# Optimization experiments

Measured on AMD Instinct MI355X. Metric: run time of the kernel, lower is better.

The kernel has to match this reference:

```python
import jax, jax.numpy as jnp
import numpy as np

IN_DIM = 128
OUT_DIM = 128
N_NEIGH = 32
BATCH = 8192


def setup_inputs() -> dict:
    key = jax.random.key(0)
    k1, k2, k3, k4, k5 = jax.random.split(key, 5)
    ai_sq = jax.random.normal(k1, (BATCH, IN_DIM), dtype=jnp.float32)
    ai_sn = jax.random.normal(k2, (N_NEIGH, BATCH, IN_DIM), dtype=jnp.float32)
    # nn.Linear params (weight [out,in], bias [out]) and attention vector u [2*out]
    W_w = jax.random.normal(k3, (OUT_DIM, IN_DIM), dtype=jnp.float32) / np.sqrt(IN_DIM)
    W_b = jax.random.normal(k4, (OUT_DIM,), dtype=jnp.float32) * 0.01
    u = jax.random.normal(k5, (2 * OUT_DIM,), dtype=jnp.float32)
    return {"ai_sq": ai_sq, "ai_sn": ai_sn, "W_w": W_w, "W_b": W_b, "u": u}


def reference(ai_sq, ai_sn, W_w, W_b, u):
    out_dim = W_w.shape[0]
    # shared linear projection W
    sq_proj = ai_sq @ W_w.T + W_b                      # [B, D]
    sn_proj = jnp.einsum('nbi,oi->nbo', ai_sn, W_w) + W_b  # [N, B, D]
    # u . concat(sq_proj, sn_proj) == u1.sq_proj + u2.sn_proj
    u1, u2 = u[:out_dim], u[out_dim:]
    mult = (sq_proj @ u1)[None, :] + jnp.einsum('nbd,d->nb', sn_proj, u2)  # [N, B]
    beta = jnp.exp(jax.nn.leaky_relu(mult, negative_slope=0.01))           # [N, B]
    return beta / jnp.sum(beta, axis=0)                # softmax-like normalize over neighbors
```

## Files before the change

### kernel.cpp

```cpp
#include <hip/hip_runtime.h>
#include <math.h>

#define IN_DIM   128
#define OUT_DIM  128
#define N_NEIGH  32
#define BATCH    8192

__global__ __launch_bounds__(128) void prep_kernel(const float* __restrict__ W_w,
                                                   const float* __restrict__ W_b,
                                                   const float* __restrict__ u,
                                                   float* __restrict__ ws) {
    int i = threadIdx.x;
    float a1 = 0.f, a2 = 0.f;
    for (int o = 0; o < OUT_DIM; ++o) {
        float w = W_w[o * IN_DIM + i];
        a1 += w * u[o];
        a2 += w * u[OUT_DIM + o];
    }
    ws[i] = a1;
    ws[IN_DIM + i] = a2;

    __shared__ float red[128];
    red[i] = W_b[i] * (u[i] + u[OUT_DIM + i]);
    __syncthreads();
    for (int s = 64; s > 0; s >>= 1) {
        if (i < s) red[i] += red[i + s];
        __syncthreads();
    }
    if (i == 0) ws[2 * IN_DIM] = red[0];
}

__global__ __launch_bounds__(256) void gat_kernel(const float* __restrict__ ai_sq,
                                                  const float* __restrict__ ai_sn,
                                                  const float* __restrict__ ws,
                                                  float* __restrict__ out) {
    const int b    = blockIdx.x;
    const int tid  = threadIdx.x;
    const int half = tid >> 5;
    const int c    = tid & 31;

    __shared__ float t[33];

    const float4* v1 = (const float4*)ws;
    const float4* v2 = (const float4*)(ws + IN_DIM);
    const float   cc = ws[2 * IN_DIM];

    const float4 v2c = v2[c];

    for (int r = half; r < 33; r += 8) {
        float4 x, vv;
        if (r < 32) {
            x  = ((const float4*)(ai_sn + ((size_t)r * BATCH + b) * IN_DIM))[c];
            vv = v2c;
        } else {
            x  = ((const float4*)(ai_sq + (size_t)b * IN_DIM))[c];
            vv = v1[c];
        }
        float p = x.x * vv.x + x.y * vv.y + x.z * vv.z + x.w * vv.w;
        for (int m = 16; m > 0; m >>= 1) p += __shfl_xor(p, m);
        if (c == 0) t[r] = p;
    }
    __syncthreads();

    if (tid < 64) {
        const int n = tid & 31;
        float mult = t[n] + t[32] + cc;
        float l = mult > 0.f ? mult : 0.01f * mult;
        float mx = l;
        for (int m = 16; m > 0; m >>= 1) mx = fmaxf(mx, __shfl_xor(mx, m));
        float e = expf(l - mx);
        float sum = e;
        for (int m = 16; m > 0; m >>= 1) sum += __shfl_xor(sum, m);
        if (tid < 32) out[(size_t)n * BATCH + b] = e / sum;
    }
}

extern "C" void kernel_launch(void* const* d_in, const int* in_sizes, int n_in,
                              void* d_out, int out_size, void* d_ws, size_t ws_size,
                              hipStream_t stream) {
    const float* ai_sq = (const float*)d_in[0];
    const float* ai_sn = (const float*)d_in[1];
    const float* W_w   = (const float*)d_in[2];
    const float* W_b   = (const float*)d_in[3];
    const float* u     = (const float*)d_in[4];
    float* out = (float*)d_out;
    float* ws  = (float*)d_ws;

    prep_kernel<<<1, 128, 0, stream>>>(W_w, W_b, u, ws);
    gat_kernel<<<BATCH, 256, 0, stream>>>(ai_sq, ai_sn, ws, out);
}
```

Baseline: 213.5 us.

## Tile eight batch rows per block and parallelize weight-vector prep

The main kernel now handles eight batch columns per block. Each wave processes two rows per pass and the results go through shared memory, so the softmax uses all threads and the output stores are grouped in runs of eight contiguous floats. The prep kernel spreads the 128-long reduction over 1024 threads with a shared-memory combine, shortening the serial tiny-kernel latency. Fewer blocks and better store coalescing trade against less parallelism per block and an extra shared-memory round trip.

Result: faster. 204.1 us (-4.4%).

```diff
diff --git a/kernel.cpp b/kernel.cpp
--- a/kernel.cpp
+++ b/kernel.cpp
@@ -5,74 +5,104 @@
 #define OUT_DIM  128
 #define N_NEIGH  32
 #define BATCH    8192
+#define B_TILE   8
 
-__global__ __launch_bounds__(128) void prep_kernel(const float* __restrict__ W_w,
-                                                   const float* __restrict__ W_b,
-                                                   const float* __restrict__ u,
-                                                   float* __restrict__ ws) {
-    int i = threadIdx.x;
+__global__ __launch_bounds__(1024) void prep_kernel(const float* __restrict__ W_w,
+                                                    const float* __restrict__ W_b,
+                                                    const float* __restrict__ u,
+                                                    float* __restrict__ ws) {
+    const int tid = threadIdx.x;
+    const int i = tid & 127;
+    const int g = tid >> 7;
+
     float a1 = 0.f, a2 = 0.f;
-    for (int o = 0; o < OUT_DIM; ++o) {
+    #pragma unroll
+    for (int oo = 0; oo < 16; ++oo) {
+        int o = g * 16 + oo;
         float w = W_w[o * IN_DIM + i];
         a1 += w * u[o];
         a2 += w * u[OUT_DIM + o];
     }
-    ws[i] = a1;
-    ws[IN_DIM + i] = a2;
+
+    __shared__ float r1[8][128];
+    __shared__ float r2[8][128];
+    r1[g][i] = a1;
+    r2[g][i] = a2;
 
     __shared__ float red[128];
-    red[i] = W_b[i] * (u[i] + u[OUT_DIM + i]);
+    if (tid < 128) red[tid] = W_b[tid] * (u[tid] + u[OUT_DIM + tid]);
     __syncthreads();
-    for (int s = 64; s > 0; s >>= 1) {
-        if (i < s) red[i] += red[i + s];
-        __syncthreads();
+
+    if (g == 0) {
+        float s1 = 0.f, s2 = 0.f;
+        #pragma unroll
+        for (int gg = 0; gg < 8; ++gg) { s1 += r1[gg][i]; s2 += r2[gg][i]; }
+        ws[i] = s1;
+        ws[IN_DIM + i] = s2;
     }
-    if (i == 0) ws[2 * IN_DIM] = red[0];
+    __syncthreads();
+    if (tid == 0) {
+        float s = 0.f;
+        for (int k = 0; k < 128; ++k) s += red[k];
+        ws[2 * IN_DIM] = s;
+    }
 }
 
 __global__ __launch_bounds__(256) void gat_kernel(const float* __restrict__ ai_sq,
                                                   const float* __restrict__ ai_sn,
                                                   const float* __restrict__ ws,
                                                   float* __restrict__ out) {
-    const int b    = blockIdx.x;
+    const int b0   = blockIdx.x * B_TILE;
     const int tid  = threadIdx.x;
-    const int half = tid >> 5;
-    const int c    = tid & 31;
+    const int wave = tid >> 6;
+    const int lane = tid & 63;
+    const int c    = lane & 31;
+    const int hb   = lane >> 5;
 
-    __shared__ float t[33];
+    __shared__ float t[33][B_TILE + 1];
 
     const float4* v1 = (const float4*)ws;
     const float4* v2 = (const float4*)(ws + IN_DIM);
     const float   cc = ws[2 * IN_DIM];
+    const float4  v1c = v1[c];
+    const float4  v2c = v2[c];
 
-    const float4 v2c = v2[c];
-
-    for (int r = half; r < 33; r += 8) {
-        float4 x, vv;
-        if (r < 32) {
-            x  = ((const float4*)(ai_sn + ((size_t)r * BATCH + b) * IN_DIM))[c];
-            vv = v2c;
-        } else {
-            x  = ((const float4*)(ai_sq + (size_t)b * IN_DIM))[c];
-            vv = v1[c];
+    for (int r = wave; r < 33; r += 4) {
+        const float* base = (r < 32)
+            ? (ai_sn + ((size_t)r * BATCH + b0) * IN_DIM)
+            : (ai_sq + (size_t)b0 * IN_DIM);
+        const float4 vv = (r < 32) ? v2c : v1c;
+        #pragma unroll
+        for (int k = 0; k < B_TILE / 2; ++k) {
+            const int bl = k * 2 + hb;
+            float4 x = ((const float4*)(base + (size_t)bl * IN_DIM))[c];
+            float p = x.x * vv.x + x.y * vv.y + x.z * vv.z + x.w * vv.w;
+            #pragma unroll
+            for (int m = 16; m > 0; m >>= 1) p += __shfl_xor(p, m);
+            if (c == 0) t[r][bl] = p;
         }
-        float p = x.x * vv.x + x.y * vv.y + x.z * vv.z + x.w * vv.w;
-        for (int m = 16; m > 0; m >>= 1) p += __shfl_xor(p, m);
-        if (c == 0) t[r] = p;
     }
     __syncthreads();
 
-    if (tid < 64) {
-        const int n = tid & 31;
-        float mult = t[n] + t[32] + cc;
-        float l = mult > 0.f ? mult : 0.01f * mult;
-        float mx = l;
-        for (int m = 16; m > 0; m >>= 1) mx = fmaxf(mx, __shfl_xor(mx, m));
-        float e = expf(l - mx);
-        float sum = e;
-        for (int m = 16; m > 0; m >>= 1) sum += __shfl_xor(sum, m);
-        if (tid < 32) out[(size_t)n * BATCH + b] = e / sum;
-    }
+    const int n  = tid & 31;
+    const int bl = tid >> 5;
+    float mult = t[n][bl] + t[32][bl] + cc;
+    float l = mult > 0.f ? mult : 0.01f * mult;
+    float mx = l;
+    #pragma unroll
+    for (int m = 16; m > 0; m >>= 1) mx = fmaxf(mx, __shfl_xor(mx, m));
+    float e = expf(l - mx);
+    float s = e;
+    #pragma unroll
+    for (int m = 16; m > 0; m >>= 1) s += __shfl_xor(s, m);
+    float res = e / s;
+    __syncthreads();
+    t[n][bl] = res;
+    __syncthreads();
+
+    const int nn = tid >> 3;
+    const int bb = tid & 7;
+    out[(size_t)nn * BATCH + b0 + bb] = t[nn][bb];
 }
 
 extern "C" void kernel_launch(void* const* d_in, const int* in_sizes, int n_in,
@@ -86,6 +116,6 @@
     float* out = (float*)d_out;
     float* ws  = (float*)d_ws;
 
-    prep_kernel<<<1, 128, 0, stream>>>(W_w, W_b, u, ws);
-    gat_kernel<<<BATCH, 256, 0, stream>>>(ai_sq, ai_sn, ws, out);
+    prep_kernel<<<1, 1024, 0, stream>>>(W_w, W_b, u, ws);
+    gat_kernel<<<BATCH / B_TILE, 256, 0, stream>>>(ai_sq, ai_sn, ws, out);
 }
```
